# Kernel optimization log

Hardware: AMD Instinct MI355X
Metric: run time of the kernel (lower is better)

Reference implementation:

```python
import jax, jax.numpy as jnp
import numpy as np

T, B, I, H = 512, 64, 512, 1024


def setup_inputs() -> dict:
    key = jax.random.key(0)
    ks = jax.random.split(key, 7)
    s = 0.03  # keep recurrent dynamics stable
    return {
        "X": jax.random.normal(ks[0], (T, B, I), jnp.float32),
        "h0": jax.random.normal(ks[1], (B, H), jnp.float32) * 0.1,
        "c0": jax.random.normal(ks[2], (B, H), jnp.float32) * 0.1,
        "Wi": jax.random.normal(ks[3], (4, I, H), jnp.float32) * s,
        "Wh": jax.random.normal(ks[4], (4, H, H), jnp.float32) * s,
        "bi": jnp.zeros((4, H), jnp.float32),
        "bh": jnp.zeros((4, H), jnp.float32),
    }


def reference(X, h0, c0, Wi, Wh, bi, bh):
    # Gate order along axis 0 of Wi/Wh/bi/bh: f, i, g, o (matches the torch module's
    # linear_if/hf, linear_ii/hi, linear_ig/hg, linear_io/ho pairs).
    b = bi + bh  # [4, H] combined bias, mathematically identical

    def step(carry, x_t):
        h, c = carry
        # z: [4, B, H] = x @ Wi_g + h @ Wh_g + b_g for each gate g
        z = (jnp.einsum('bi,gih->gbh', x_t, Wi)
             + jnp.einsum('bh,ghk->gbk', h, Wh)
             + b[:, None, :])
        f = jax.nn.sigmoid(z[0])
        i = jax.nn.sigmoid(z[1])
        g = jnp.tanh(z[2])
        o = jax.nn.sigmoid(z[3])
        c_new = f * c + i * g
        h_new = o * jnp.tanh(c_new)
        return (h_new, c_new), h_new

    (h_n, c_n), outputs = jax.lax.scan(step, (h0, c0), X)
    return outputs, h_n, c_n
```

## Files before the change

### kernel.cpp

```cpp
#include <hip/hip_runtime.h>
#include <stdint.h>

#define T_STEPS 512
#define NB 64
#define NI 512
#define NH 1024
#define NBLK 128
#define DEPTH 32

typedef __attribute__((ext_vector_type(8))) short short8;
typedef __attribute__((ext_vector_type(4))) float floatx4;
typedef __attribute__((ext_vector_type(16))) float floatx16;
typedef __attribute__((ext_vector_type(4))) unsigned short ushortx4;

__device__ __forceinline__ unsigned short f2bf(float f) {
  union { float f; uint32_t u; } v; v.f = f;
  return (unsigned short)((v.u + 0x7FFFu + ((v.u >> 16) & 1u)) >> 16);
}
__device__ __forceinline__ float bf2f(unsigned short s) {
  union { uint32_t u; float f; } v; v.u = ((uint32_t)s) << 16; return v.f;
}
__device__ __forceinline__ float sigmoid_f(float x) {
  return 1.0f / (1.0f + __expf(-x));
}
__device__ __forceinline__ float tanh_f(float x) {
  float xx = fminf(fmaxf(x, -15.0f), 15.0f);
  float e = __expf(2.0f * xx);
  return (e - 1.0f) / (e + 1.0f);
}


__global__ void convert_x(const float* __restrict__ X, unsigned short* __restrict__ Xb) {
  int i = blockIdx.x * 256 + threadIdx.x;
  floatx4 x = ((const floatx4*)X)[i];
  ushortx4 o;
  o[0] = f2bf(x[0]); o[1] = f2bf(x[1]); o[2] = f2bf(x[2]); o[3] = f2bf(x[3]);
  ((ushortx4*)Xb)[i] = o;
}

__global__ void transpose_bf16(const float* __restrict__ in, unsigned short* __restrict__ outp,
                               int K, int N) {
  __shared__ float tile[64][65];
  int g = blockIdx.z;
  int k0 = blockIdx.x * 64, n0 = blockIdx.y * 64;
  int tx = threadIdx.x & 63, ty = threadIdx.x >> 6;
  const float* src = in + (size_t)g * K * N;
  unsigned short* dst = outp + (size_t)g * K * N;
#pragma unroll
  for (int i = 0; i < 16; i++) {
    int r = ty * 16 + i;
    tile[r][tx] = src[(size_t)(k0 + r) * N + n0 + tx];
  }
  __syncthreads();
#pragma unroll
  for (int i = 0; i < 16; i++) {
    int r = ty * 16 + i;
    dst[(size_t)(n0 + r) * K + k0 + tx] = f2bf(tile[tx][r]);
  }
}

__global__ void prep_small(const float* __restrict__ bi, const float* __restrict__ bh,
                           const float* __restrict__ h0, float* __restrict__ bias,
                           unsigned short* __restrict__ hbuf0, unsigned* __restrict__ flags) {
  int i = blockIdx.x * 256 + threadIdx.x;
  if (i < NBLK) flags[i] = 0u;
  if (i < 4 * NH) bias[i] = bi[i] + bh[i];
  if (i < NB * NH) hbuf0[i] = f2bf(h0[i]);
}

__global__ __launch_bounds__(256) void gemm_zx(
    const unsigned short* __restrict__ Xb,
    const unsigned short* __restrict__ WibT,
    const float* __restrict__ bias,
    unsigned short* __restrict__ Zq) {
  __shared__ __align__(16) unsigned short As[128][40];
  __shared__ __align__(16) unsigned short Bs[128][40];
  __shared__ __align__(16) unsigned short stg[16384];
  const int g = blockIdx.z;
  const int m0 = blockIdx.x * 128;
  const int n0 = blockIdx.y * 128;
  const int tid = threadIdx.x;
  const int lane = tid & 63;
  const int wave = tid >> 6;
  const int wm = wave & 1, wn = wave >> 1;
  const int fr = lane & 15;
  const int fq = (lane >> 4) * 8;

  const unsigned short* Bsrc = WibT + (size_t)g * NH * NI;

  floatx4 acc[4][4];
#pragma unroll
  for (int a = 0; a < 4; a++)
#pragma unroll
    for (int b = 0; b < 4; b++)
#pragma unroll
      for (int z = 0; z < 4; z++) acc[a][b][z] = 0.0f;

  for (int k0 = 0; k0 < NI; k0 += 32) {
#pragma unroll
    for (int it = 0; it < 2; it++) {
      int c = tid + it * 256;
      int row = c >> 2, kc = (c & 3) * 8;
      *(uint4*)(&As[row][kc]) = *(const uint4*)(Xb + (size_t)(m0 + row) * NI + k0 + kc);
      *(uint4*)(&Bs[row][kc]) = *(const uint4*)(Bsrc + (size_t)(n0 + row) * NI + k0 + kc);
    }
    __syncthreads();
    short8 af[4], bf[4];
#pragma unroll
    for (int ms = 0; ms < 4; ms++) af[ms] = *(const short8*)(&As[wm * 64 + ms * 16 + fr][fq]);
#pragma unroll
    for (int ns = 0; ns < 4; ns++) bf[ns] = *(const short8*)(&Bs[wn * 64 + ns * 16 + fr][fq]);
#pragma unroll
    for (int ms = 0; ms < 4; ms++)
#pragma unroll
      for (int ns = 0; ns < 4; ns++)
        acc[ms][ns] = __builtin_amdgcn_mfma_f32_16x16x32_bf16(af[ms], bf[ns], acc[ms][ns], 0, 0, 0);
    __syncthreads();
  }

#pragma unroll
  for (int ns = 0; ns < 4; ns++) {
    int jrel = wn * 64 + ns * 16 + fr;
    float bs = bias[g * NH + n0 + jrel];
    int bkp = jrel >> 3, jj = jrel & 7;
#pragma unroll
    for (int ms = 0; ms < 4; ms++) {
#pragma unroll
      for (int r = 0; r < 4; r++) {
        int mrel = wm * 64 + ms * 16 + (lane >> 4) * 4 + r;
        int tp = mrel >> 6, b = mrel & 63;
        int wm2 = b >> 5, row32 = b & 31;
        int half2 = (row32 >> 2) & 1;
        int rr = (row32 & 3) | ((row32 >> 3) << 2);
        int idx = (((((tp * 16 + bkp) * 2 + wm2) * 2 + half2) * 8 + jj) * 16) + rr;
        stg[idx] = f2bf(acc[ms][ns][r] + bs);
      }
    }
  }
  __syncthreads();
  const size_t t0 = (size_t)(m0 >> 6);
  const int bk0 = n0 >> 3;
#pragma unroll
  for (int tp = 0; tp < 2; tp++) {
    size_t gbase = (((t0 + tp) * 4 + g) * 128 + bk0) * 512;
#pragma unroll
    for (int c = 0; c < 4; c++) {
      int e = c * 2048 + tid * 8;
      *(uint4*)(Zq + gbase + e) = *(const uint4*)(stg + tp * 8192 + e);
    }
  }
}


template<int C>
__device__ __forceinline__ void load_a_c(const unsigned short* ap, short8 (&areg)[64]) {
  asm volatile("global_load_dwordx4 %0, %1, off offset:%2 sc0 sc1"
               : "=v"(areg[C]) : "v"(ap), "i"(C * 32));
}

template<int C>
__device__ __forceinline__ void load_b_c(const unsigned short* bfr, int lane, short8 (&bs)[64]) {
  bs[C] = *(const short8*)(&bfr[((size_t)(C * 64) + lane) * 8]);
}

template<int S, int I>
struct PrologR {
  static __device__ __forceinline__ void run(const unsigned short* ap, short8 (&areg)[64]) {
    load_a_c<(S + I) & 63>(ap, areg);
    PrologR<S, I + 1>::run(ap, areg);
  }
};
template<int S>
struct PrologR<S, DEPTH> {
  static __device__ __forceinline__ void run(const unsigned short*, short8 (&)[64]) {}
};

template<int S, int I>
struct ChunksR {
  static __device__ __forceinline__ void run(const unsigned short* ap, const unsigned short* bfr,
                                             int lane, short8 (&areg)[64], short8 (&bs)[64],
                                             floatx16& acc0, floatx16& acc1) {
    if constexpr (I + DEPTH < 64) load_a_c<(S + I + DEPTH) & 63>(ap, areg);
    if constexpr (I + 4 < 64) load_b_c<(S + I + 4) & 63>(bfr, lane, bs);
    constexpr int NOUT = (I + DEPTH < 64) ? DEPTH : (63 - I);
    constexpr int C = (S + I) & 63;
    asm volatile("s_waitcnt vmcnt(%1)" : "+v"(areg[C]) : "i"(NOUT) : "memory");
    if constexpr ((I & 1) == 0)
      acc0 = __builtin_amdgcn_mfma_f32_32x32x16_bf16(areg[C], bs[C], acc0, 0, 0, 0);
    else
      acc1 = __builtin_amdgcn_mfma_f32_32x32x16_bf16(areg[C], bs[C], acc1, 0, 0, 0);
    ChunksR<S, I + 1>::run(ap, bfr, lane, areg, bs, acc0, acc1);
  }
};
template<int S>
struct ChunksR<S, 64> {
  static __device__ __forceinline__ void run(const unsigned short*, const unsigned short*,
                                             int, short8 (&)[64], short8 (&)[64],
                                             floatx16&, floatx16&) {}
};

template<int S>
__device__ __forceinline__ void lstm_step(
    int t, const unsigned short* __restrict__ Zq, unsigned short* __restrict__ hbuf,
    unsigned* __restrict__ flags, float* __restrict__ out,
    const unsigned short* bfr, const unsigned long long* fpq,
    int tid, int lane, int wm, int nl, int g0, int jj, int half, int bk, int j0,
    size_t zoff, const int (&brow)[16], float (&creg)[16],
    uint4 (&zc)[2], uint4 (&zn)[2]) {
  const int hsz = NB * NH;

  if (t) {
    unsigned tgt = (unsigned)t;
    for (;;) {
      unsigned long long fv = __hip_atomic_load(fpq, __ATOMIC_RELAXED,
                                                __HIP_MEMORY_SCOPE_AGENT);
      unsigned a = (unsigned)fv, b2 = (unsigned)(fv >> 32);
      if (__all((int)((a >= tgt) && (b2 >= tgt)))) break;
      __builtin_amdgcn_s_sleep(1);
    }
  }
  asm volatile("s_waitcnt vmcnt(0)" ::: "memory");
  __builtin_amdgcn_sched_barrier(0);

  const unsigned short* hin = hbuf + (size_t)(t & 1) * hsz;
  unsigned short* hout = hbuf + (size_t)((t + 1) & 1) * hsz;
  const unsigned short* ap = hin + (size_t)(wm * 32 + nl) * NH + half * 8;

  floatx16 acc0, acc1;
#pragma unroll
  for (int z = 0; z < 16; z++) { acc0[z] = 0.0f; acc1[z] = 0.0f; }

  short8 areg[64];
  short8 bs[64];
  PrologR<S, 0>::run(ap, areg);
  load_b_c<(S + 0) & 63>(bfr, lane, bs);
  load_b_c<(S + 1) & 63>(bfr, lane, bs);
  load_b_c<(S + 2) & 63>(bfr, lane, bs);
  load_b_c<(S + 3) & 63>(bfr, lane, bs);
  ChunksR<S, 0>::run(ap, bfr, lane, areg, bs, acc0, acc1);
  __builtin_amdgcn_sched_barrier(0);

#pragma unroll
  for (int z = 0; z < 16; z++) acc0[z] += acc1[z];

  unsigned zd[8];
  zd[0] = zc[0].x; zd[1] = zc[0].y; zd[2] = zc[0].z; zd[3] = zc[0].w;
  zd[4] = zc[1].x; zd[5] = zc[1].y; zd[6] = zc[1].z; zd[7] = zc[1].w;

  float harr[16];
#pragma unroll
  for (int r = 0; r < 16; r++) {
    unsigned dw = zd[r >> 1];
    float zxv = bf2f((unsigned short)((r & 1) ? (dw >> 16) : (dw & 0xffffu)));
    float z0 = acc0[r] + zxv;
    float z1 = __shfl_xor(z0, 8);
    float z2 = __shfl_xor(z0, 16);
    float z3 = __shfl_xor(z1, 16);
    bool bb0 = (g0 & 1) != 0, bb1 = (g0 & 2) != 0;
    float zf = bb1 ? (bb0 ? z3 : z2) : (bb0 ? z1 : z0);
    float zi = bb1 ? (bb0 ? z2 : z3) : (bb0 ? z0 : z1);
    float zg = bb1 ? (bb0 ? z1 : z0) : (bb0 ? z3 : z2);
    float zo = bb1 ? (bb0 ? z0 : z1) : (bb0 ? z2 : z3);
    float fg = sigmoid_f(zf);
    float ig = sigmoid_f(zi);
    float gg = tanh_f(zg);
    float og = sigmoid_f(zo);
    float c = fg * creg[r] + ig * gg;
    creg[r] = c;
    float h = og * tanh_f(c);
    harr[r] = h;
    if (g0 == 0) {
      __hip_atomic_store(&hout[(size_t)brow[r] * NH + j0 + jj], f2bf(h),
                         __ATOMIC_RELAXED, __HIP_MEMORY_SCOPE_AGENT);
    }
  }

  if (t + 1 < T_STEPS) {
    asm volatile("s_waitcnt vmcnt(0)" ::: "memory");
    __syncthreads();
    if (tid == 0)
      __hip_atomic_store(flags + bk, (unsigned)(t + 1),
                         __ATOMIC_RELAXED, __HIP_MEMORY_SCOPE_AGENT);
    const unsigned short* zp = Zq + (size_t)(t + 1) * 262144 + zoff;
    asm volatile("global_load_dwordx4 %0, %1, off nt" : "=v"(zn[0]) : "v"(zp));
    asm volatile("global_load_dwordx4 %0, %1, off offset:16 nt" : "=v"(zn[1]) : "v"(zp));
  }

  if (g0 == 0) {
#pragma unroll
    for (int r = 0; r < 16; r++) {
      size_t oidx = (size_t)brow[r] * NH + j0 + jj;
      __builtin_nontemporal_store(harr[r], &out[(size_t)t * hsz + oidx]);
      if (t == T_STEPS - 1)
        __builtin_nontemporal_store(harr[r], &out[(size_t)T_STEPS * hsz + oidx]);
    }
  }
}

template<int S>
__device__ __forceinline__ void lstm_loop(
    const unsigned short* __restrict__ Zq, unsigned short* __restrict__ hbuf,
    unsigned* __restrict__ flags, float* __restrict__ out,
    const unsigned short* bfr, const unsigned long long* fpq,
    int tid, int lane, int wm, int nl, int g0, int jj, int half, int bk, int j0,
    size_t zoff, const int (&brow)[16], float (&creg)[16]) {
  uint4 zA[2], zB[2];
  {
    const unsigned short* zp = Zq + zoff;
    asm volatile("global_load_dwordx4 %0, %1, off nt" : "=v"(zA[0]) : "v"(zp));
    asm volatile("global_load_dwordx4 %0, %1, off offset:16 nt" : "=v"(zA[1]) : "v"(zp));
  }
  for (int t2 = 0; t2 < T_STEPS; t2 += 2) {
    lstm_step<S>(t2,     Zq, hbuf, flags, out, bfr, fpq, tid, lane, wm, nl, g0, jj,
                 half, bk, j0, zoff, brow, creg, zA, zB);
    lstm_step<S>(t2 + 1, Zq, hbuf, flags, out, bfr, fpq, tid, lane, wm, nl, g0, jj,
                 half, bk, j0, zoff, brow, creg, zB, zA);
  }
}

__global__ __launch_bounds__(128, 1) void lstm_persist(
    const unsigned short* __restrict__ Zq,
    const unsigned short* __restrict__ WhT,
    const float* __restrict__ c0,
    unsigned short* __restrict__ hbuf,
    unsigned* __restrict__ flags,
    float* __restrict__ out) {
  __shared__ __align__(16) unsigned short bfr[64 * 64 * 8];

  const int bk = blockIdx.x;
  const int j0 = bk * 8;
  const int tid = threadIdx.x;
  const int lane = tid & 63;
  const int wm = tid >> 6;
  const int nl = lane & 31;
  const int g0 = nl >> 3;
  const int jj = nl & 7;
  const int half = lane >> 5;

  for (int i = 0; i < 32; i++) {
    int f = tid + i * 128;
    int fl = f & 63, kk = f >> 6;
    int n = fl & 31;
    size_t wrow = (size_t)((n >> 3) * NH + j0 + (n & 7));
    int kb = kk * 16 + (fl >> 5) * 8;
    uint4 v = *(const uint4*)(WhT + wrow * NH + kb);
    *(uint4*)(&bfr[(size_t)f * 8]) = v;
  }

  float creg[16];
  int brow[16];
#pragma unroll
  for (int r = 0; r < 16; r++) {
    brow[r] = wm * 32 + (r & 3) + 8 * (r >> 2) + 4 * half;
    creg[r] = c0[(size_t)brow[r] * NH + j0 + jj];
  }
  __syncthreads();

  const unsigned long long* fpq = (const unsigned long long*)flags + lane;
  const size_t zoff = (((((size_t)g0 * 128 + bk) * 2 + wm) * 2 + half) * 8 + jj) * 16;

  switch (bk & 3) {
    case 0: lstm_loop<0>(Zq, hbuf, flags, out, bfr, fpq, tid, lane, wm, nl, g0, jj,
                         half, bk, j0, zoff, brow, creg); break;
    case 1: lstm_loop<16>(Zq, hbuf, flags, out, bfr, fpq, tid, lane, wm, nl, g0, jj,
                          half, bk, j0, zoff, brow, creg); break;
    case 2: lstm_loop<32>(Zq, hbuf, flags, out, bfr, fpq, tid, lane, wm, nl, g0, jj,
                          half, bk, j0, zoff, brow, creg); break;
    default: lstm_loop<48>(Zq, hbuf, flags, out, bfr, fpq, tid, lane, wm, nl, g0, jj,
                           half, bk, j0, zoff, brow, creg); break;
  }

  if (g0 == 0) {
#pragma unroll
    for (int r = 0; r < 16; r++)
      __builtin_nontemporal_store(
          creg[r], &out[(size_t)T_STEPS * NB * NH + NB * NH + (size_t)brow[r] * NH + j0 + jj]);
  }
}

extern "C" void kernel_launch(void* const* d_in, const int* in_sizes, int n_in,
                              void* d_out, int out_size, void* d_ws, size_t ws_size,
                              hipStream_t stream) {
  const float* X  = (const float*)d_in[0];
  const float* h0 = (const float*)d_in[1];
  const float* c0 = (const float*)d_in[2];
  const float* Wi = (const float*)d_in[3];
  const float* Wh = (const float*)d_in[4];
  const float* bi = (const float*)d_in[5];
  const float* bh = (const float*)d_in[6];
  float* out = (float*)d_out;

  uint8_t* ws = (uint8_t*)d_ws;
  size_t off = 0;
  auto alloc = [&](size_t bytes) -> void* {
    void* p = ws + off;
    off += (bytes + 255) & ~(size_t)255;
    return p;
  };
  unsigned short* Zq   = (unsigned short*)alloc((size_t)T_STEPS * NB * 4096 * 2);
  unsigned short* Xb   = (unsigned short*)alloc((size_t)T_STEPS * NB * NI * 2);
  unsigned short* WibT = (unsigned short*)alloc((size_t)4 * NH * NI * 2);
  unsigned short* WhT  = (unsigned short*)alloc((size_t)4 * NH * NH * 2);
  float* bias          = (float*)alloc((size_t)4 * NH * 4);
  unsigned short* hbuf = (unsigned short*)alloc((size_t)2 * NB * NH * 2);
  unsigned* flags      = (unsigned*)alloc((size_t)NBLK * 32 * 4);

  if (off > ws_size) {
    hipMemsetAsync(d_out, 0x7F, (size_t)out_size * 4, stream);
    return;
  }

  convert_x<<<16384, 256, 0, stream>>>(X, Xb);
  transpose_bf16<<<dim3(8, 16, 4), 256, 0, stream>>>(Wi, WibT, NI, NH);
  transpose_bf16<<<dim3(16, 16, 4), 256, 0, stream>>>(Wh, WhT, NH, NH);
  prep_small<<<256, 256, 0, stream>>>(bi, bh, h0, bias, hbuf, flags);
  gemm_zx<<<dim3(256, 8, 4), 256, 0, stream>>>(Xb, WibT, bias, Zq);

  lstm_persist<<<dim3(NBLK), dim3(128), 0, stream>>>(Zq, WhT, c0, hbuf, flags, out);
}
```

Before: 5.881 ms.

## Halve persistent LSTM blocks, each computing two hidden-column tiles per step

New measurement: 16.11 ms. 174% more time.

```diff
diff --git a/kernel.cpp b/kernel.cpp
--- a/kernel.cpp
+++ b/kernel.cpp
@@ -5,13 +5,14 @@
 #define NB 64
 #define NI 512
 #define NH 1024
-#define NBLK 128
-#define DEPTH 32
+#define NBLK 64
+#define DEPTH 16
 
 typedef __attribute__((ext_vector_type(8))) short short8;
 typedef __attribute__((ext_vector_type(4))) float floatx4;
 typedef __attribute__((ext_vector_type(16))) float floatx16;
 typedef __attribute__((ext_vector_type(4))) unsigned short ushortx4;
+typedef __attribute__((ext_vector_type(4))) unsigned int uintx4;
 
 __device__ __forceinline__ unsigned short f2bf(float f) {
   union { float f; uint32_t u; } v; v.f = f;
@@ -27,6 +28,9 @@
   float xx = fminf(fmaxf(x, -15.0f), 15.0f);
   float e = __expf(2.0f * xx);
   return (e - 1.0f) / (e + 1.0f);
+}
+__device__ __forceinline__ uintx4 ntload4(const unsigned short* p) {
+  return __builtin_nontemporal_load((const uintx4*)p);
 }
 
 
@@ -63,7 +67,7 @@
                            const float* __restrict__ h0, float* __restrict__ bias,
                            unsigned short* __restrict__ hbuf0, unsigned* __restrict__ flags) {
   int i = blockIdx.x * 256 + threadIdx.x;
-  if (i < NBLK) flags[i] = 0u;
+  if (i < 4096) flags[i] = 0u;
   if (i < 4 * NH) bias[i] = bi[i] + bh[i];
   if (i < NB * NH) hbuf0[i] = f2bf(h0[i]);
 }
@@ -158,9 +162,9 @@
                : "=v"(areg[C]) : "v"(ap), "i"(C * 32));
 }
 
-template<int C>
+template<int C, int T>
 __device__ __forceinline__ void load_b_c(const unsigned short* bfr, int lane, short8 (&bs)[64]) {
-  bs[C] = *(const short8*)(&bfr[((size_t)(C * 64) + lane) * 8]);
+  bs[C] = *(const short8*)(&bfr[((size_t)((T * 64 + C) * 64) + lane) * 8]);
 }
 
 template<int S, int I>
@@ -178,46 +182,49 @@
 template<int S, int I>
 struct ChunksR {
   static __device__ __forceinline__ void run(const unsigned short* ap, const unsigned short* bfr,
-                                             int lane, short8 (&areg)[64], short8 (&bs)[64],
+                                             int lane, short8 (&areg)[64],
+                                             short8 (&bs0)[64], short8 (&bs1)[64],
                                              floatx16& acc0, floatx16& acc1) {
     if constexpr (I + DEPTH < 64) load_a_c<(S + I + DEPTH) & 63>(ap, areg);
-    if constexpr (I + 4 < 64) load_b_c<(S + I + 4) & 63>(bfr, lane, bs);
+    if constexpr (I + 2 < 64) {
+      load_b_c<(S + I + 2) & 63, 0>(bfr, lane, bs0);
+      load_b_c<(S + I + 2) & 63, 1>(bfr, lane, bs1);
+    }
     constexpr int NOUT = (I + DEPTH < 64) ? DEPTH : (63 - I);
     constexpr int C = (S + I) & 63;
     asm volatile("s_waitcnt vmcnt(%1)" : "+v"(areg[C]) : "i"(NOUT) : "memory");
-    if constexpr ((I & 1) == 0)
-      acc0 = __builtin_amdgcn_mfma_f32_32x32x16_bf16(areg[C], bs[C], acc0, 0, 0, 0);
-    else
-      acc1 = __builtin_amdgcn_mfma_f32_32x32x16_bf16(areg[C], bs[C], acc1, 0, 0, 0);
-    ChunksR<S, I + 1>::run(ap, bfr, lane, areg, bs, acc0, acc1);
+    acc0 = __builtin_amdgcn_mfma_f32_32x32x16_bf16(areg[C], bs0[C], acc0, 0, 0, 0);
+    acc1 = __builtin_amdgcn_mfma_f32_32x32x16_bf16(areg[C], bs1[C], acc1, 0, 0, 0);
+    ChunksR<S, I + 1>::run(ap, bfr, lane, areg, bs0, bs1, acc0, acc1);
   }
 };
 template<int S>
 struct ChunksR<S, 64> {
   static __device__ __forceinline__ void run(const unsigned short*, const unsigned short*,
                                              int, short8 (&)[64], short8 (&)[64],
-                                             floatx16&, floatx16&) {}
+                                             short8 (&)[64], floatx16&, floatx16&) {}
 };
 
 template<int S>
 __device__ __forceinline__ void lstm_step(
     int t, const unsigned short* __restrict__ Zq, unsigned short* __restrict__ hbuf,
     unsigned* __restrict__ flags, float* __restrict__ out,
-    const unsigned short* bfr, const unsigned long long* fpq,
+    const unsigned short* bfr, const unsigned* fp,
     int tid, int lane, int wm, int nl, int g0, int jj, int half, int bk, int j0,
-    size_t zoff, const int (&brow)[16], float (&creg)[16],
-    uint4 (&zc)[2], uint4 (&zn)[2]) {
+    size_t zoff, const int (&brow)[16], float (&creg0)[16], float (&creg1)[16]) {
   const int hsz = NB * NH;
+
+  const unsigned short* zp = Zq + (size_t)t * 262144 + zoff;
+  uintx4 zq0 = ntload4(zp);
+  uintx4 zq1 = ntload4(zp + 8);
+  uintx4 zq2 = ntload4(zp + 512);
+  uintx4 zq3 = ntload4(zp + 520);
 
   if (t) {
     unsigned tgt = (unsigned)t;
-    for (;;) {
-      unsigned long long fv = __hip_atomic_load(fpq, __ATOMIC_RELAXED,
-                                                __HIP_MEMORY_SCOPE_AGENT);
-      unsigned a = (unsigned)fv, b2 = (unsigned)(fv >> 32);
-      if (__all((int)((a >= tgt) && (b2 >= tgt)))) break;
+    while (!__all((int)(__hip_atomic_load(fp, __ATOMIC_RELAXED,
+                                          __HIP_MEMORY_SCOPE_AGENT) >= tgt)))
       __builtin_amdgcn_s_sleep(1);
-    }
   }
   asm volatile("s_waitcnt vmcnt(0)" ::: "memory");
   __builtin_amdgcn_sched_barrier(0);
@@ -231,26 +238,25 @@
   for (int z = 0; z < 16; z++) { acc0[z] = 0.0f; acc1[z] = 0.0f; }
 
   short8 areg[64];
-  short8 bs[64];
+  short8 bs0[64], bs1[64];
   PrologR<S, 0>::run(ap, areg);
-  load_b_c<(S + 0) & 63>(bfr, lane, bs);
-  load_b_c<(S + 1) & 63>(bfr, lane, bs);
-  load_b_c<(S + 2) & 63>(bfr, lane, bs);
-  load_b_c<(S + 3) & 63>(bfr, lane, bs);
-  ChunksR<S, 0>::run(ap, bfr, lane, areg, bs, acc0, acc1);
+  load_b_c<(S + 0) & 63, 0>(bfr, lane, bs0);
+  load_b_c<(S + 0) & 63, 1>(bfr, lane, bs1);
+  load_b_c<(S + 1) & 63, 0>(bfr, lane, bs0);
+  load_b_c<(S + 1) & 63, 1>(bfr, lane, bs1);
+  ChunksR<S, 0>::run(ap, bfr, lane, areg, bs0, bs1, acc0, acc1);
   __builtin_amdgcn_sched_barrier(0);
 
-#pragma unroll
-  for (int z = 0; z < 16; z++) acc0[z] += acc1[z];
-
-  unsigned zd[8];
-  zd[0] = zc[0].x; zd[1] = zc[0].y; zd[2] = zc[0].z; zd[3] = zc[0].w;
-  zd[4] = zc[1].x; zd[5] = zc[1].y; zd[6] = zc[1].z; zd[7] = zc[1].w;
-
-  float harr[16];
+  unsigned zd0[8], zd1[8];
+  zd0[0] = zq0[0]; zd0[1] = zq0[1]; zd0[2] = zq0[2]; zd0[3] = zq0[3];
+  zd0[4] = zq1[0]; zd0[5] = zq1[1]; zd0[6] = zq1[2]; zd0[7] = zq1[3];
+  zd1[0] = zq2[0]; zd1[1] = zq2[1]; zd1[2] = zq2[2]; zd1[3] = zq2[3];
+  zd1[4] = zq3[0]; zd1[5] = zq3[1]; zd1[6] = zq3[2]; zd1[7] = zq3[3];
+
+  float h0arr[16], h1arr[16];
 #pragma unroll
   for (int r = 0; r < 16; r++) {
-    unsigned dw = zd[r >> 1];
+    unsigned dw = zd0[r >> 1];
     float zxv = bf2f((unsigned short)((r & 1) ? (dw >> 16) : (dw & 0xffffu)));
     float z0 = acc0[r] + zxv;
     float z1 = __shfl_xor(z0, 8);
@@ -261,18 +267,36 @@
     float zi = bb1 ? (bb0 ? z2 : z3) : (bb0 ? z0 : z1);
     float zg = bb1 ? (bb0 ? z1 : z0) : (bb0 ? z3 : z2);
     float zo = bb1 ? (bb0 ? z0 : z1) : (bb0 ? z2 : z3);
-    float fg = sigmoid_f(zf);
-    float ig = sigmoid_f(zi);
-    float gg = tanh_f(zg);
-    float og = sigmoid_f(zo);
-    float c = fg * creg[r] + ig * gg;
-    creg[r] = c;
+    float fg = sigmoid_f(zf), ig = sigmoid_f(zi), gg = tanh_f(zg), og = sigmoid_f(zo);
+    float c = fg * creg0[r] + ig * gg;
+    creg0[r] = c;
     float h = og * tanh_f(c);
-    harr[r] = h;
-    if (g0 == 0) {
+    h0arr[r] = h;
+    if (g0 == 0)
       __hip_atomic_store(&hout[(size_t)brow[r] * NH + j0 + jj], f2bf(h),
                          __ATOMIC_RELAXED, __HIP_MEMORY_SCOPE_AGENT);
-    }
+  }
+#pragma unroll
+  for (int r = 0; r < 16; r++) {
+    unsigned dw = zd1[r >> 1];
+    float zxv = bf2f((unsigned short)((r & 1) ? (dw >> 16) : (dw & 0xffffu)));
+    float z0 = acc1[r] + zxv;
+    float z1 = __shfl_xor(z0, 8);
+    float z2 = __shfl_xor(z0, 16);
+    float z3 = __shfl_xor(z1, 16);
+    bool bb0 = (g0 & 1) != 0, bb1 = (g0 & 2) != 0;
+    float zf = bb1 ? (bb0 ? z3 : z2) : (bb0 ? z1 : z0);
+    float zi = bb1 ? (bb0 ? z2 : z3) : (bb0 ? z0 : z1);
+    float zg = bb1 ? (bb0 ? z1 : z0) : (bb0 ? z3 : z2);
+    float zo = bb1 ? (bb0 ? z0 : z1) : (bb0 ? z2 : z3);
+    float fg = sigmoid_f(zf), ig = sigmoid_f(zi), gg = tanh_f(zg), og = sigmoid_f(zo);
+    float c = fg * creg1[r] + ig * gg;
+    creg1[r] = c;
+    float h = og * tanh_f(c);
+    h1arr[r] = h;
+    if (g0 == 0)
+      __hip_atomic_store(&hout[(size_t)brow[r] * NH + j0 + 8 + jj], f2bf(h),
+                         __ATOMIC_RELAXED, __HIP_MEMORY_SCOPE_AGENT);
   }
 
   if (t + 1 < T_STEPS) {
@@ -281,18 +305,19 @@
     if (tid == 0)
       __hip_atomic_store(flags + bk, (unsigned)(t + 1),
                          __ATOMIC_RELAXED, __HIP_MEMORY_SCOPE_AGENT);
-    const unsigned short* zp = Zq + (size_t)(t + 1) * 262144 + zoff;
-    asm volatile("global_load_dwordx4 %0, %1, off nt" : "=v"(zn[0]) : "v"(zp));
-    asm volatile("global_load_dwordx4 %0, %1, off offset:16 nt" : "=v"(zn[1]) : "v"(zp));
   }
 
   if (g0 == 0) {
 #pragma unroll
     for (int r = 0; r < 16; r++) {
-      size_t oidx = (size_t)brow[r] * NH + j0 + jj;
-      __builtin_nontemporal_store(harr[r], &out[(size_t)t * hsz + oidx]);
-      if (t == T_STEPS - 1)
-        __builtin_nontemporal_store(harr[r], &out[(size_t)T_STEPS * hsz + oidx]);
+      size_t obase = (size_t)t * hsz + (size_t)brow[r] * NH + j0;
+      out[obase + jj] = h0arr[r];
+      out[obase + 8 + jj] = h1arr[r];
+      if (t == T_STEPS - 1) {
+        size_t nbase = (size_t)T_STEPS * hsz + (size_t)brow[r] * NH + j0;
+        out[nbase + jj] = h0arr[r];
+        out[nbase + 8 + jj] = h1arr[r];
+      }
     }
   }
 }
@@ -301,20 +326,12 @@
 __device__ __forceinline__ void lstm_loop(
     const unsigned short* __restrict__ Zq, unsigned short* __restrict__ hbuf,
     unsigned* __restrict__ flags, float* __restrict__ out,
-    const unsigned short* bfr, const unsigned long long* fpq,
+    const unsigned short* bfr, const unsigned* fp,
     int tid, int lane, int wm, int nl, int g0, int jj, int half, int bk, int j0,
-    size_t zoff, const int (&brow)[16], float (&creg)[16]) {
-  uint4 zA[2], zB[2];
-  {
-    const unsigned short* zp = Zq + zoff;
-    asm volatile("global_load_dwordx4 %0, %1, off nt" : "=v"(zA[0]) : "v"(zp));
-    asm volatile("global_load_dwordx4 %0, %1, off offset:16 nt" : "=v"(zA[1]) : "v"(zp));
-  }
-  for (int t2 = 0; t2 < T_STEPS; t2 += 2) {
-    lstm_step<S>(t2,     Zq, hbuf, flags, out, bfr, fpq, tid, lane, wm, nl, g0, jj,
-                 half, bk, j0, zoff, brow, creg, zA, zB);
-    lstm_step<S>(t2 + 1, Zq, hbuf, flags, out, bfr, fpq, tid, lane, wm, nl, g0, jj,
-                 half, bk, j0, zoff, brow, creg, zB, zA);
+    size_t zoff, const int (&brow)[16], float (&creg0)[16], float (&creg1)[16]) {
+  for (int t = 0; t < T_STEPS; t++) {
+    lstm_step<S>(t, Zq, hbuf, flags, out, bfr, fp, tid, lane, wm, nl, g0, jj,
+                 half, bk, j0, zoff, brow, creg0, creg1);
   }
 }
 
@@ -325,10 +342,10 @@
     unsigned short* __restrict__ hbuf,
     unsigned* __restrict__ flags,
     float* __restrict__ out) {
-  __shared__ __align__(16) unsigned short bfr[64 * 64 * 8];
+  __shared__ __align__(16) unsigned short bfr[2 * 64 * 64 * 8];
 
   const int bk = blockIdx.x;
-  const int j0 = bk * 8;
+  const int j0 = bk * 16;
   const int tid = threadIdx.x;
   const int lane = tid & 63;
   const int wm = tid >> 6;
@@ -337,44 +354,49 @@
   const int jj = nl & 7;
   const int half = lane >> 5;
 
-  for (int i = 0; i < 32; i++) {
+  for (int i = 0; i < 64; i++) {
     int f = tid + i * 128;
-    int fl = f & 63, kk = f >> 6;
+    int c = f >> 12, rem = f & 4095;
+    int kk = rem >> 6, fl = rem & 63;
     int n = fl & 31;
-    size_t wrow = (size_t)((n >> 3) * NH + j0 + (n & 7));
+    size_t wrow = (size_t)(n >> 3) * NH + j0 + c * 8 + (n & 7);
     int kb = kk * 16 + (fl >> 5) * 8;
     uint4 v = *(const uint4*)(WhT + wrow * NH + kb);
     *(uint4*)(&bfr[(size_t)f * 8]) = v;
   }
 
-  float creg[16];
+  float creg0[16], creg1[16];
   int brow[16];
 #pragma unroll
   for (int r = 0; r < 16; r++) {
     brow[r] = wm * 32 + (r & 3) + 8 * (r >> 2) + 4 * half;
-    creg[r] = c0[(size_t)brow[r] * NH + j0 + jj];
+    creg0[r] = c0[(size_t)brow[r] * NH + j0 + jj];
+    creg1[r] = c0[(size_t)brow[r] * NH + j0 + 8 + jj];
   }
   __syncthreads();
 
-  const unsigned long long* fpq = (const unsigned long long*)flags + lane;
-  const size_t zoff = (((((size_t)g0 * 128 + bk) * 2 + wm) * 2 + half) * 8 + jj) * 16;
+  const unsigned* fp = flags + lane;
+  const size_t zoff =
+      (((((size_t)g0 * 128 + 2 * bk) * 2 + wm) * 2 + half) * 8 + jj) * 16;
 
   switch (bk & 3) {
-    case 0: lstm_loop<0>(Zq, hbuf, flags, out, bfr, fpq, tid, lane, wm, nl, g0, jj,
-                         half, bk, j0, zoff, brow, creg); break;
-    case 1: lstm_loop<16>(Zq, hbuf, flags, out, bfr, fpq, tid, lane, wm, nl, g0, jj,
-                          half, bk, j0, zoff, brow, creg); break;
-    case 2: lstm_loop<32>(Zq, hbuf, flags, out, bfr, fpq, tid, lane, wm, nl, g0, jj,
-                          half, bk, j0, zoff, brow, creg); break;
-    default: lstm_loop<48>(Zq, hbuf, flags, out, bfr, fpq, tid, lane, wm, nl, g0, jj,
-                           half, bk, j0, zoff, brow, creg); break;
+    case 0: lstm_loop<0>(Zq, hbuf, flags, out, bfr, fp, tid, lane, wm, nl, g0, jj,
+                         half, bk, j0, zoff, brow, creg0, creg1); break;
+    case 1: lstm_loop<16>(Zq, hbuf, flags, out, bfr, fp, tid, lane, wm, nl, g0, jj,
+                          half, bk, j0, zoff, brow, creg0, creg1); break;
+    case 2: lstm_loop<32>(Zq, hbuf, flags, out, bfr, fp, tid, lane, wm, nl, g0, jj,
+                          half, bk, j0, zoff, brow, creg0, creg1); break;
+    default: lstm_loop<48>(Zq, hbuf, flags, out, bfr, fp, tid, lane, wm, nl, g0, jj,
+                           half, bk, j0, zoff, brow, creg0, creg1); break;
   }
 
   if (g0 == 0) {
 #pragma unroll
-    for (int r = 0; r < 16; r++)
-      __builtin_nontemporal_store(
-          creg[r], &out[(size_t)T_STEPS * NB * NH + NB * NH + (size_t)brow[r] * NH + j0 + jj]);
+    for (int r = 0; r < 16; r++) {
+      size_t nbase = (size_t)T_STEPS * NB * NH + NB * NH + (size_t)brow[r] * NH + j0;
+      out[nbase + jj] = creg0[r];
+      out[nbase + 8 + jj] = creg1[r];
+    }
   }
 }
 
@@ -403,7 +425,7 @@
   unsigned short* WhT  = (unsigned short*)alloc((size_t)4 * NH * NH * 2);
   float* bias          = (float*)alloc((size_t)4 * NH * 4);
   unsigned short* hbuf = (unsigned short*)alloc((size_t)2 * NB * NH * 2);
-  unsigned* flags      = (unsigned*)alloc((size_t)NBLK * 32 * 4);
+  unsigned* flags      = (unsigned*)alloc((size_t)4096 * 4);
 
   if (off > ws_size) {
     hipMemsetAsync(d_out, 0x7F, (size_t)out_size * 4, stream);
```
